# Kernel optimization log

Measured on AMD Instinct MI355X. Metric: run time of the kernel, lower is better.

Reference implementation:

```python
import jax, jax.numpy as jnp
import numpy as np

D_MODEL = 1024
D_STATE = 16
D_CONV = 4
EXPAND = 2
D_INNER = EXPAND * D_MODEL          # 2048
DT_RANK = D_INNER // 16             # 128
BATCH = 2
SEQLEN = 1024


def _silu(x):
    return x * jax.nn.sigmoid(x)


def setup_inputs() -> dict:
    key = jax.random.key(0)
    ks = jax.random.split(key, 8)
    s = 0.02
    A_init = jnp.tile(jnp.arange(1, D_STATE + 1, dtype=jnp.float32)[None, :], (D_INNER, 1))
    return {
        "x": jax.random.normal(ks[0], (BATCH, SEQLEN, D_MODEL), jnp.float32),
        "W_in": jax.random.normal(ks[1], (D_MODEL, 2 * D_INNER), jnp.float32) * s,
        "conv_k": jax.random.normal(ks[2], (D_CONV, 1, D_INNER), jnp.float32) * s,  # (kw, in/groups, out)
        "conv_b": jnp.zeros((D_INNER,), jnp.float32),
        "W_xproj": jax.random.normal(ks[3], (D_INNER, DT_RANK + 2 * D_STATE), jnp.float32) * s,
        "W_dt": jax.random.normal(ks[4], (DT_RANK, D_INNER), jnp.float32) * s,
        "b_dt": jnp.zeros((D_INNER,), jnp.float32),
        "A_log": jnp.log(A_init),
        "D": jnp.ones((D_INNER,), jnp.float32),
        "W_out": jax.random.normal(ks[5], (D_INNER, D_MODEL), jnp.float32) * s,
    }


def reference(x, W_in, conv_k, conv_b, W_xproj, W_dt, b_dt, A_log, D, W_out):
    # in_proj and gate split
    xz = x @ W_in                                   # (B, L, 2*Di)
    x_in, z = jnp.split(xz, 2, axis=-1)             # each (B, L, Di)

    # depthwise causal conv1d: left-pad by d_conv-1 (keras padding='causal')
    xp = jnp.pad(x_in, ((0, 0), (D_CONV - 1, 0), (0, 0)))
    x_in = jax.lax.conv_general_dilated(
        xp, conv_k, window_strides=(1,), padding='VALID',
        dimension_numbers=('NWC', 'WIO', 'NWC'),
        feature_group_count=D_INNER) + conv_b
    u = _silu(x_in)                                 # (B, L, Di)

    # input-dependent SSM params
    x_dbl = u @ W_xproj                             # (B, L, dt_rank + 2*N)
    dt_low, Bm, Cm = jnp.split(x_dbl, [DT_RANK, DT_RANK + D_STATE], axis=-1)
    dt = jax.nn.softplus(dt_low @ W_dt + b_dt)      # (B, L, Di)
    A = -jnp.exp(A_log)                             # (Di, N)
    dA = jnp.exp(jnp.einsum('bld,dn->bldn', dt, A)) # (B, L, Di, N)
    dB = jnp.einsum('bld,bln->bldn', dt, Bm)        # (B, L, Di, N)

    # selective scan over sequence length
    def step(h, e):
        a_t, b_t, u_t, c_t = e                      # (B,Di,N), (B,Di,N), (B,Di), (B,N)
        h = a_t * h + b_t * u_t[..., None]
        y_t = jnp.einsum('bdn,bn->bd', h, c_t)
        return h, y_t

    h0 = jnp.zeros((x.shape[0], D_INNER, D_STATE), dtype=x.dtype)
    xs = (jnp.swapaxes(dA, 0, 1), jnp.swapaxes(dB, 0, 1),
          jnp.swapaxes(u, 0, 1), jnp.swapaxes(Cm, 0, 1))
    _, yT = jax.lax.scan(step, h0, xs)              # (L, B, Di)
    y = jnp.swapaxes(yT, 0, 1) + u * D              # skip connection

    return (y * _silu(z)) @ W_out                   # (B, L, d_model)
```

## Files before the change

kernel.cpp:

```cpp
#include <hip/hip_runtime.h>
#include <hip/hip_bf16.h>

#define D_MODEL 1024
#define D_STATE 16
#define D_CONV 4
#define D_INNER 2048
#define DT_RANK 128
#define BATCH 2
#define SEQLEN 1024
#define XCOLS 160
#define NCHUNK 64
#define LCHUNK 16

typedef __hip_bfloat16 bf16;
typedef __attribute__((ext_vector_type(8))) short short8;
typedef __attribute__((ext_vector_type(4))) float f32x4;

__device__ __forceinline__ unsigned short f2bf_bits(float f) {
    bf16 h = __float2bfloat16(f);
    return *(unsigned short*)&h;
}

__device__ __forceinline__ float softplus_f(float x) {
    return fmaxf(x, 0.f) + __logf(1.f + __expf(-fabsf(x)));
}

__device__ __forceinline__ void load16_lds(void* lds, const void* g) {
    __builtin_amdgcn_global_load_lds(
        (const __attribute__((address_space(1))) unsigned int*)g,
        (__attribute__((address_space(3))) unsigned int*)lds, 16, 0, 0);
}

__device__ __forceinline__ void transpose_tile(const float* __restrict__ B,
                                               bf16* __restrict__ Bt,
                                               int K, int N, int nt, int kt,
                                               float (*t)[33], int tid)
{
    const int tx = tid & 31, ty = tid >> 5;
    const int n0 = nt * 32, k0 = kt * 32;
    #pragma unroll
    for (int r = 0; r < 4; ++r) {
        int n = n0 + tx;
        t[ty + r * 8][tx] = (n < N) ? B[(size_t)(k0 + ty + r * 8) * N + n] : 0.f;
    }
    __syncthreads();
    #pragma unroll
    for (int r = 0; r < 4; ++r)
        Bt[(size_t)(n0 + ty + r * 8) * K + k0 + tx] = __float2bfloat16(t[tx][ty + r * 8]);
}

__global__ __launch_bounds__(256)
void prep_kernel(const float* __restrict__ x, bf16* __restrict__ x_bf,
                 const float* __restrict__ W_in, bf16* __restrict__ Win_t,
                 const float* __restrict__ W_xproj, bf16* __restrict__ Wxp_t,
                 const float* __restrict__ W_dt, bf16* __restrict__ Wdt_t,
                 const float* __restrict__ W_out, bf16* __restrict__ Wout_t,
                 const float* __restrict__ A_log, float* __restrict__ Aneg)
{
    __shared__ float t[32][33];
    const int tid = threadIdx.x;
    int blk = blockIdx.x;
    if (blk < 4096) {
        transpose_tile(W_in, Win_t, D_MODEL, 2 * D_INNER, blk & 127, blk >> 7, t, tid);
        return;
    }
    blk -= 4096;
    if (blk < 512) {
        transpose_tile(W_xproj, Wxp_t, D_INNER, XCOLS, blk & 7, blk >> 3, t, tid);
        return;
    }
    blk -= 512;
    if (blk < 256) {
        transpose_tile(W_dt, Wdt_t, DT_RANK, D_INNER, blk & 63, blk >> 6, t, tid);
        return;
    }
    blk -= 256;
    if (blk < 2048) {
        transpose_tile(W_out, Wout_t, D_INNER, D_MODEL, blk & 31, blk >> 5, t, tid);
        return;
    }
    blk -= 2048;
    if (blk < 2048) {
        int i = blk * 256 + tid;
        float4 v = ((const float4*)x)[i];
        ushort4 p;
        p.x = f2bf_bits(v.x); p.y = f2bf_bits(v.y);
        p.z = f2bf_bits(v.z); p.w = f2bf_bits(v.w);
        ((ushort4*)x_bf)[i] = p;
        return;
    }
    blk -= 2048;
    {
        int i = blk * 256 + tid;
        Aneg[i] = -__expf(A_log[i]);
    }
}

template<int BN, int EPI>
__global__ __launch_bounds__(256)
void gemm_mfma(const bf16* __restrict__ A, const bf16* __restrict__ Bt,
               float* __restrict__ C, bf16* __restrict__ Cb,
               const float* __restrict__ bias,
               int M, int N, int K, int ldc, int kchunk)
{
    constexpr int WN = (BN == 128) ? 64 : 32;
    constexpr int NJ = WN / 16;
    __shared__ short As[128 * 32];
    __shared__ short Bs[BN * 32];
    const int tid = threadIdx.x;
    const int lane = tid & 63, wave = tid >> 6;
    const int wm = (wave >> 1) * 64, wn = (wave & 1) * WN;
    const int row0 = blockIdx.y * 128, col0 = blockIdx.x * BN;
    const int r_m = lane & 15, r_q = lane >> 4;
    const int kstart = blockIdx.z * kchunk;
    float* Cz = C + (size_t)blockIdx.z * M * ldc;

    const int srow = tid >> 2, schk = (tid & 3) * 8;
    const bf16* Ag0 = A  + (size_t)(row0 + srow)      * K + kstart + schk;
    const bf16* Ag1 = A  + (size_t)(row0 + srow + 64) * K + kstart + schk;
    const bf16* Bg0 = Bt + (size_t)(col0 + srow)      * K + kstart + schk;
    const bf16* Bg1 = Bt + (size_t)(col0 + srow + 64) * K + kstart + schk;
    short* AsW0 = &As[8 * tid];
    short* AsW1 = &As[8 * tid + 2048];
    short* BsW0 = &Bs[8 * tid];
    short* BsW1 = &Bs[8 * tid + 2048];

    f32x4 acc[4][NJ];
    #pragma unroll
    for (int i = 0; i < 4; ++i)
        #pragma unroll
        for (int j = 0; j < NJ; ++j)
            #pragma unroll
            for (int r = 0; r < 4; ++r) acc[i][j][r] = 0.f;

    for (int k0 = 0; k0 < kchunk; k0 += 32) {
        __syncthreads();
        load16_lds(AsW0, Ag0 + k0);
        load16_lds(AsW1, Ag1 + k0);
        load16_lds(BsW0, Bg0 + k0);
        if (BN == 128) load16_lds(BsW1, Bg1 + k0);
        __syncthreads();
        short8 af[4], bfr[NJ];
        #pragma unroll
        for (int i = 0; i < 4; ++i)
            af[i] = *(const short8*)&As[(wm + i * 16 + r_m) * 32 + r_q * 8];
        #pragma unroll
        for (int j = 0; j < NJ; ++j)
            bfr[j] = *(const short8*)&Bs[(wn + j * 16 + r_m) * 32 + r_q * 8];
        #pragma unroll
        for (int i = 0; i < 4; ++i)
            #pragma unroll
            for (int j = 0; j < NJ; ++j)
                acc[i][j] = __builtin_amdgcn_mfma_f32_16x16x32_bf16(
                    af[i], bfr[j], acc[i][j], 0, 0, 0);
    }

    #pragma unroll
    for (int i = 0; i < 4; ++i) {
        #pragma unroll
        for (int j = 0; j < NJ; ++j) {
            int row = row0 + wm + i * 16 + r_q * 4;
            int col = col0 + wn + j * 16 + r_m;
            if (col < N) {
                if (EPI == 1) {
                    float bv = bias[col];
                    #pragma unroll
                    for (int r = 0; r < 4; ++r)
                        Cb[(size_t)(row + r) * ldc + col] =
                            __float2bfloat16(softplus_f(acc[i][j][r] + bv));
                } else {
                    #pragma unroll
                    for (int r = 0; r < 4; ++r)
                        Cz[(size_t)(row + r) * ldc + col] = acc[i][j][r];
                }
            }
        }
    }
}

__global__ __launch_bounds__(256)
void reduce_xdbl(const float* __restrict__ Cpart, float* __restrict__ x_dbl,
                 bf16* __restrict__ dtA_bf)
{
    int i = blockIdx.x * 256 + threadIdx.x;
    if (i >= 2048 * XCOLS) return;
    int r = i / XCOLS, c = i - r * XCOLS;
    float s = 0.f;
    #pragma unroll
    for (int z = 0; z < 8; ++z)
        s += Cpart[(size_t)z * 2048 * 256 + (size_t)r * 256 + c];
    x_dbl[i] = s;
    if (c < DT_RANK) dtA_bf[(size_t)r * DT_RANK + c] = __float2bfloat16(s);
}

__global__ __launch_bounds__(256)
void reduce_out(const float* __restrict__ Cpart, float* __restrict__ out)
{
    int i = blockIdx.x * 256 + threadIdx.x;
    const float4* p0 = (const float4*)Cpart;
    const float4* p1 = p0 + (size_t)2048 * 1024 / 4;
    float4 a = p0[i], b = p1[i];
    float4 r; r.x = a.x + b.x; r.y = a.y + b.y; r.z = a.z + b.z; r.w = a.w + b.w;
    ((float4*)out)[i] = r;
}

__global__ __launch_bounds__(256)
void conv_silu_kernel(const float* __restrict__ xz,
                      const float* __restrict__ conv_k,
                      const float* __restrict__ conv_b,
                      bf16* __restrict__ u_bf)
{
    int idx4 = blockIdx.x * 256 + threadIdx.x;
    int d4 = idx4 & (D_INNER / 4 - 1);
    int t = (idx4 >> 9) & (SEQLEN - 1);
    int b = idx4 >> 19;
    float4 acc = ((const float4*)conv_b)[d4];
    #pragma unroll
    for (int k = 0; k < D_CONV; ++k) {
        int tt = t + k - (D_CONV - 1);
        if (tt >= 0) {
            float4 xv = ((const float4*)xz)[(size_t)(b * SEQLEN + tt) * (2 * D_INNER / 4) + d4];
            float4 kv = ((const float4*)conv_k)[k * (D_INNER / 4) + d4];
            acc.x = fmaf(xv.x, kv.x, acc.x);
            acc.y = fmaf(xv.y, kv.y, acc.y);
            acc.z = fmaf(xv.z, kv.z, acc.z);
            acc.w = fmaf(xv.w, kv.w, acc.w);
        }
    }
    ushort4 pk;
    pk.x = f2bf_bits(acc.x / (1.f + __expf(-acc.x)));
    pk.y = f2bf_bits(acc.y / (1.f + __expf(-acc.y)));
    pk.z = f2bf_bits(acc.z / (1.f + __expf(-acc.z)));
    pk.w = f2bf_bits(acc.w / (1.f + __expf(-acc.w)));
    ((ushort4*)u_bf)[idx4] = pk;
}

__global__ __launch_bounds__(256)
void scan_phase1(const bf16* __restrict__ dt_sb,
                 const float* __restrict__ Aneg,
                 const bf16* __restrict__ u_bf,
                 const float* __restrict__ x_dbl,
                 float* __restrict__ Pst, float* __restrict__ Sst)
{
    __shared__ float Bsm[LCHUNK][16];
    const int d = blockIdx.x * 256 + threadIdx.x;
    const int c = blockIdx.y, b = blockIdx.z;
    const int t0 = c * LCHUNK;
    {
        int tt = threadIdx.x >> 4, n = threadIdx.x & 15;
        Bsm[tt][n] = x_dbl[(size_t)(b * SEQLEN + t0 + tt) * XCOLS + DT_RANK + n];
    }
    float A_row[D_STATE];
    const float4* a4 = (const float4*)(Aneg + d * D_STATE);
    #pragma unroll
    for (int q = 0; q < 4; ++q) {
        float4 v = a4[q];
        A_row[q*4+0] = v.x; A_row[q*4+1] = v.y; A_row[q*4+2] = v.z; A_row[q*4+3] = v.w;
    }
    __syncthreads();
    float P[D_STATE], S[D_STATE];
    #pragma unroll
    for (int n = 0; n < D_STATE; ++n) { P[n] = 1.f; S[n] = 0.f; }
    const bf16* dpp = dt_sb + (size_t)(b * SEQLEN + t0) * D_INNER + d;
    const bf16* upp = u_bf + (size_t)(b * SEQLEN + t0) * D_INNER + d;
    #pragma unroll
    for (int t = 0; t < LCHUNK; ++t) {
        float dtv = __bfloat162float(dpp[(size_t)t * D_INNER]);
        float du = dtv * __bfloat162float(upp[(size_t)t * D_INNER]);
        const float4* b4 = (const float4*)&Bsm[t][0];
        #pragma unroll
        for (int q = 0; q < 4; ++q) {
            float4 v = b4[q];
            float Bn[4] = {v.x, v.y, v.z, v.w};
            #pragma unroll
            for (int e = 0; e < 4; ++e) {
                int n = q * 4 + e;
                float a = __expf(dtv * A_row[n]);
                P[n] *= a;
                S[n] = fmaf(a, S[n], du * Bn[e]);
            }
        }
    }
    const size_t base = ((size_t)(b * NCHUNK + c) * D_STATE) * D_INNER + d;
    #pragma unroll
    for (int n = 0; n < D_STATE; ++n) {
        Pst[base + (size_t)n * D_INNER] = P[n];
        Sst[base + (size_t)n * D_INNER] = S[n];
    }
}

__global__ __launch_bounds__(256)
void scan_phase2(const float* __restrict__ Pst, float* __restrict__ Sst)
{
    const int d = blockIdx.x * 256 + threadIdx.x;
    const int n = blockIdx.y;
    const int b = blockIdx.z;
    float h = 0.f;
    for (int c = 0; c < NCHUNK; ++c) {
        const size_t idx = ((size_t)(b * NCHUNK + c) * D_STATE + n) * D_INNER + d;
        float Pv = Pst[idx], Sv = Sst[idx];
        Sst[idx] = h;
        h = fmaf(Pv, h, Sv);
    }
}

__global__ __launch_bounds__(256)
void scan_phase3(const bf16* __restrict__ dt_sb,
                 const float* __restrict__ Aneg,
                 const bf16* __restrict__ u_bf,
                 const float* __restrict__ x_dbl,
                 const float* __restrict__ Dvec,
                 const float* __restrict__ xz,
                 const float* __restrict__ hin,
                 bf16* __restrict__ g_bf)
{
    __shared__ float BCs[LCHUNK][32];
    const int d = blockIdx.x * 256 + threadIdx.x;
    const int c = blockIdx.y, b = blockIdx.z;
    const int t0 = c * LCHUNK;
    {
        int i0 = threadIdx.x;
        int tt = i0 >> 5, col = i0 & 31;
        BCs[tt][col] = x_dbl[(size_t)(b * SEQLEN + t0 + tt) * XCOLS + DT_RANK + col];
        int i1 = i0 + 256;
        tt = i1 >> 5; col = i1 & 31;
        BCs[tt][col] = x_dbl[(size_t)(b * SEQLEN + t0 + tt) * XCOLS + DT_RANK + col];
    }
    float A_row[D_STATE];
    const float4* a4 = (const float4*)(Aneg + d * D_STATE);
    #pragma unroll
    for (int q = 0; q < 4; ++q) {
        float4 v = a4[q];
        A_row[q*4+0] = v.x; A_row[q*4+1] = v.y; A_row[q*4+2] = v.z; A_row[q*4+3] = v.w;
    }
    const float Dd = Dvec[d];
    __syncthreads();
    float h[D_STATE];
    const size_t base = ((size_t)(b * NCHUNK + c) * D_STATE) * D_INNER + d;
    #pragma unroll
    for (int n = 0; n < D_STATE; ++n) h[n] = hin[base + (size_t)n * D_INNER];
    const bf16* dpp = dt_sb + (size_t)(b * SEQLEN + t0) * D_INNER + d;
    const bf16* upp = u_bf + (size_t)(b * SEQLEN + t0) * D_INNER + d;
    const float* zpp = xz + (size_t)(b * SEQLEN + t0) * (2 * D_INNER) + D_INNER + d;
    bf16* gpp = g_bf + (size_t)(b * SEQLEN + t0) * D_INNER + d;
    #pragma unroll
    for (int t = 0; t < LCHUNK; ++t) {
        float dtv = __bfloat162float(dpp[(size_t)t * D_INNER]);
        float uv = __bfloat162float(upp[(size_t)t * D_INNER]);
        float zv = zpp[(size_t)t * 2 * D_INNER];
        float du = dtv * uv;
        float y = 0.f;
        const float4* bc4 = (const float4*)&BCs[t][0];
        #pragma unroll
        for (int q = 0; q < 4; ++q) {
            float4 v = bc4[q];
            float4 w = bc4[q + 4];
            float Bn[4] = {v.x, v.y, v.z, v.w};
            float Cn[4] = {w.x, w.y, w.z, w.w};
            #pragma unroll
            for (int e = 0; e < 4; ++e) {
                int n = q * 4 + e;
                float a = __expf(dtv * A_row[n]);
                h[n] = fmaf(a, h[n], du * Bn[e]);
                y = fmaf(h[n], Cn[e], y);
            }
        }
        float gy = y + uv * Dd;
        float sz = zv / (1.f + __expf(-zv));
        gpp[(size_t)t * D_INNER] = __float2bfloat16(gy * sz);
    }
}

extern "C" void kernel_launch(void* const* d_in, const int* in_sizes, int n_in,
                              void* d_out, int out_size, void* d_ws, size_t ws_size,
                              hipStream_t stream)
{
    const float* x      = (const float*)d_in[0];
    const float* W_in   = (const float*)d_in[1];
    const float* conv_k = (const float*)d_in[2];
    const float* conv_b = (const float*)d_in[3];
    const float* W_xproj= (const float*)d_in[4];
    const float* W_dt   = (const float*)d_in[5];
    const float* b_dt   = (const float*)d_in[6];
    const float* A_log  = (const float*)d_in[7];
    const float* Dvec   = (const float*)d_in[8];
    const float* W_out  = (const float*)d_in[9];
    float* out = (float*)d_out;

    const int BL = BATCH * SEQLEN;

    float* ws     = (float*)d_ws;
    float* xz     = ws;
    float* x_dbl  = xz     + (size_t)BL * 2 * D_INNER;
    float* Pst    = x_dbl  + (size_t)BL * XCOLS;
    float* Sst    = Pst    + (size_t)BATCH * NCHUNK * D_STATE * D_INNER;
    float* Aneg   = Sst    + (size_t)BATCH * NCHUNK * D_STATE * D_INNER;
    float* Cpart3 = Pst;
    float* Cpart6 = Pst;
    bf16*  x_bf   = (bf16*)Sst;
    bf16* Win_t  = (bf16*)(Aneg + 32768);
    bf16* u_bf   = Win_t + (size_t)4096 * 1024;
    bf16* Wxp_t  = u_bf  + (size_t)BL * D_INNER;
    bf16* dtA_bf = Wxp_t + (size_t)256 * 2048;
    bf16* Wdt_t  = dtA_bf+ (size_t)BL * DT_RANK;
    bf16* g_bf   = Wdt_t + (size_t)2048 * 128;
    bf16* Wout_t = g_bf  + (size_t)BL * D_INNER;
    bf16* dt_sb  = Wout_t+ (size_t)1024 * 2048;

    prep_kernel<<<4096 + 512 + 256 + 2048 + 2048 + 128, 256, 0, stream>>>(
        x, x_bf, W_in, Win_t, W_xproj, Wxp_t, W_dt, Wdt_t, W_out, Wout_t, A_log, Aneg);

    gemm_mfma<128, 0><<<dim3(32, 16, 1), 256, 0, stream>>>(
        x_bf, Win_t, xz, nullptr, nullptr, BL, 2 * D_INNER, D_MODEL, 2 * D_INNER, D_MODEL);

    conv_silu_kernel<<<(BL * D_INNER / 4) / 256, 256, 0, stream>>>(xz, conv_k, conv_b, u_bf);

    gemm_mfma<64, 0><<<dim3(4, 16, 8), 256, 0, stream>>>(
        u_bf, Wxp_t, Cpart3, nullptr, nullptr, BL, 256, D_INNER, 256, 256);
    reduce_xdbl<<<(BL * XCOLS + 255) / 256, 256, 0, stream>>>(Cpart3, x_dbl, dtA_bf);

    gemm_mfma<64, 1><<<dim3(32, 16, 1), 256, 0, stream>>>(
        dtA_bf, Wdt_t, nullptr, dt_sb, b_dt, BL, D_INNER, DT_RANK, D_INNER, DT_RANK);

    scan_phase1<<<dim3(D_INNER / 256, NCHUNK, BATCH), 256, 0, stream>>>(
        dt_sb, Aneg, u_bf, x_dbl, Pst, Sst);
    scan_phase2<<<dim3(D_INNER / 256, D_STATE, BATCH), 256, 0, stream>>>(Pst, Sst);
    scan_phase3<<<dim3(D_INNER / 256, NCHUNK, BATCH), 256, 0, stream>>>(
        dt_sb, Aneg, u_bf, x_dbl, Dvec, xz, Sst, g_bf);

    gemm_mfma<64, 0><<<dim3(16, 16, 2), 256, 0, stream>>>(
        g_bf, Wout_t, Cpart6, nullptr, nullptr, BL, D_MODEL, D_INNER, D_MODEL, D_MODEL);
    reduce_out<<<(BL * D_MODEL / 4) / 256, 256, 0, stream>>>(Cpart6, out);
}
```

Before: 234.7 us.

## Fuse z-gate SiLU into in_proj epilogue and retune scan chunks and split-K

```diff
diff --git a/kernel.cpp b/kernel.cpp
--- a/kernel.cpp
+++ b/kernel.cpp
@@ -9,8 +9,8 @@
 #define BATCH 2
 #define SEQLEN 1024
 #define XCOLS 160
-#define NCHUNK 64
-#define LCHUNK 16
+#define NCHUNK 32
+#define LCHUNK 32
 
 typedef __hip_bfloat16 bf16;
 typedef __attribute__((ext_vector_type(8))) short short8;
@@ -23,6 +23,10 @@
 
 __device__ __forceinline__ float softplus_f(float x) {
     return fmaxf(x, 0.f) + __logf(1.f + __expf(-fabsf(x)));
+}
+
+__device__ __forceinline__ float silu_f(float x) {
+    return x / (1.f + __expf(-x));
 }
 
 __device__ __forceinline__ void load16_lds(void* lds, const void* g) {
@@ -168,6 +172,18 @@
                     for (int r = 0; r < 4; ++r)
                         Cb[(size_t)(row + r) * ldc + col] =
                             __float2bfloat16(softplus_f(acc[i][j][r] + bv));
+                } else if (EPI == 2) {
+                    if (col < 2048) {
+                        #pragma unroll
+                        for (int r = 0; r < 4; ++r)
+                            Cz[(size_t)(row + r) * ldc + col] = acc[i][j][r];
+                    } else {
+                        int zc = col - 2048;
+                        #pragma unroll
+                        for (int r = 0; r < 4; ++r)
+                            Cb[(size_t)(row + r) * ldc + zc] =
+                                __float2bfloat16(silu_f(acc[i][j][r]));
+                    }
                 } else {
                     #pragma unroll
                     for (int r = 0; r < 4; ++r)
@@ -197,15 +213,19 @@
 void reduce_out(const float* __restrict__ Cpart, float* __restrict__ out)
 {
     int i = blockIdx.x * 256 + threadIdx.x;
-    const float4* p0 = (const float4*)Cpart;
-    const float4* p1 = p0 + (size_t)2048 * 1024 / 4;
-    float4 a = p0[i], b = p1[i];
-    float4 r; r.x = a.x + b.x; r.y = a.y + b.y; r.z = a.z + b.z; r.w = a.w + b.w;
+    const size_t stride = (size_t)2048 * 1024 / 4;
+    const float4* p = (const float4*)Cpart;
+    float4 a = p[i], b = p[i + stride], c = p[i + 2 * stride], d = p[i + 3 * stride];
+    float4 r;
+    r.x = (a.x + b.x) + (c.x + d.x);
+    r.y = (a.y + b.y) + (c.y + d.y);
+    r.z = (a.z + b.z) + (c.z + d.z);
+    r.w = (a.w + b.w) + (c.w + d.w);
     ((float4*)out)[i] = r;
 }
 
 __global__ __launch_bounds__(256)
-void conv_silu_kernel(const float* __restrict__ xz,
+void conv_silu_kernel(const float* __restrict__ x_lin,
                       const float* __restrict__ conv_k,
                       const float* __restrict__ conv_b,
                       bf16* __restrict__ u_bf)
@@ -219,7 +239,7 @@
     for (int k = 0; k < D_CONV; ++k) {
         int tt = t + k - (D_CONV - 1);
         if (tt >= 0) {
-            float4 xv = ((const float4*)xz)[(size_t)(b * SEQLEN + tt) * (2 * D_INNER / 4) + d4];
+            float4 xv = ((const float4*)x_lin)[(size_t)(b * SEQLEN + tt) * (D_INNER / 4) + d4];
             float4 kv = ((const float4*)conv_k)[k * (D_INNER / 4) + d4];
             acc.x = fmaf(xv.x, kv.x, acc.x);
             acc.y = fmaf(xv.y, kv.y, acc.y);
@@ -246,8 +266,8 @@
     const int d = blockIdx.x * 256 + threadIdx.x;
     const int c = blockIdx.y, b = blockIdx.z;
     const int t0 = c * LCHUNK;
-    {
-        int tt = threadIdx.x >> 4, n = threadIdx.x & 15;
+    for (int i = threadIdx.x; i < LCHUNK * 16; i += 256) {
+        int tt = i >> 4, n = i & 15;
         Bsm[tt][n] = x_dbl[(size_t)(b * SEQLEN + t0 + tt) * XCOLS + DT_RANK + n];
     }
     float A_row[D_STATE];
@@ -263,7 +283,7 @@
     for (int n = 0; n < D_STATE; ++n) { P[n] = 1.f; S[n] = 0.f; }
     const bf16* dpp = dt_sb + (size_t)(b * SEQLEN + t0) * D_INNER + d;
     const bf16* upp = u_bf + (size_t)(b * SEQLEN + t0) * D_INNER + d;
-    #pragma unroll
+    #pragma unroll 8
     for (int t = 0; t < LCHUNK; ++t) {
         float dtv = __bfloat162float(dpp[(size_t)t * D_INNER]);
         float du = dtv * __bfloat162float(upp[(size_t)t * D_INNER]);
@@ -310,7 +330,7 @@
                  const bf16* __restrict__ u_bf,
                  const float* __restrict__ x_dbl,
                  const float* __restrict__ Dvec,
-                 const float* __restrict__ xz,
+                 const bf16* __restrict__ sz_bf,
                  const float* __restrict__ hin,
                  bf16* __restrict__ g_bf)
 {
@@ -318,12 +338,8 @@
     const int d = blockIdx.x * 256 + threadIdx.x;
     const int c = blockIdx.y, b = blockIdx.z;
     const int t0 = c * LCHUNK;
-    {
-        int i0 = threadIdx.x;
-        int tt = i0 >> 5, col = i0 & 31;
-        BCs[tt][col] = x_dbl[(size_t)(b * SEQLEN + t0 + tt) * XCOLS + DT_RANK + col];
-        int i1 = i0 + 256;
-        tt = i1 >> 5; col = i1 & 31;
+    for (int i = threadIdx.x; i < LCHUNK * 32; i += 256) {
+        int tt = i >> 5, col = i & 31;
         BCs[tt][col] = x_dbl[(size_t)(b * SEQLEN + t0 + tt) * XCOLS + DT_RANK + col];
     }
     float A_row[D_STATE];
@@ -341,13 +357,13 @@
     for (int n = 0; n < D_STATE; ++n) h[n] = hin[base + (size_t)n * D_INNER];
     const bf16* dpp = dt_sb + (size_t)(b * SEQLEN + t0) * D_INNER + d;
     const bf16* upp = u_bf + (size_t)(b * SEQLEN + t0) * D_INNER + d;
-    const float* zpp = xz + (size_t)(b * SEQLEN + t0) * (2 * D_INNER) + D_INNER + d;
+    const bf16* zpp = sz_bf + (size_t)(b * SEQLEN + t0) * D_INNER + d;
     bf16* gpp = g_bf + (size_t)(b * SEQLEN + t0) * D_INNER + d;
-    #pragma unroll
+    #pragma unroll 8
     for (int t = 0; t < LCHUNK; ++t) {
         float dtv = __bfloat162float(dpp[(size_t)t * D_INNER]);
         float uv = __bfloat162float(upp[(size_t)t * D_INNER]);
-        float zv = zpp[(size_t)t * 2 * D_INNER];
+        float sz = __bfloat162float(zpp[(size_t)t * D_INNER]);
         float du = dtv * uv;
         float y = 0.f;
         const float4* bc4 = (const float4*)&BCs[t][0];
@@ -366,7 +382,6 @@
             }
         }
         float gy = y + uv * Dd;
-        float sz = zv / (1.f + __expf(-zv));
         gpp[(size_t)t * D_INNER] = __float2bfloat16(gy * sz);
     }
 }
@@ -390,17 +405,17 @@
     const int BL = BATCH * SEQLEN;
 
     float* ws     = (float*)d_ws;
-    float* xz     = ws;
-    float* x_dbl  = xz     + (size_t)BL * 2 * D_INNER;
-    float* Pst    = x_dbl  + (size_t)BL * XCOLS;
-    float* Sst    = Pst    + (size_t)BATCH * NCHUNK * D_STATE * D_INNER;
-    float* Aneg   = Sst    + (size_t)BATCH * NCHUNK * D_STATE * D_INNER;
-    float* Cpart3 = Pst;
-    float* Cpart6 = Pst;
-    bf16*  x_bf   = (bf16*)Sst;
-    bf16* Win_t  = (bf16*)(Aneg + 32768);
+    float* x_lin  = ws;
+    float* x_dbl  = x_lin + (size_t)BL * D_INNER;
+    float* Pst    = x_dbl + (size_t)BL * XCOLS;
+    float* Sst    = Pst + (size_t)BATCH * NCHUNK * D_STATE * D_INNER;
+    float* Aneg   = Sst + (size_t)BATCH * NCHUNK * D_STATE * D_INNER;
+    float* Cpart  = Aneg + 32768;
+    bf16*  x_bf   = (bf16*)Cpart;
+    bf16* Win_t  = (bf16*)(Cpart + (size_t)4 * 2048 * 1024);
     bf16* u_bf   = Win_t + (size_t)4096 * 1024;
-    bf16* Wxp_t  = u_bf  + (size_t)BL * D_INNER;
+    bf16* sz_bf  = u_bf  + (size_t)BL * D_INNER;
+    bf16* Wxp_t  = sz_bf + (size_t)BL * D_INNER;
     bf16* dtA_bf = Wxp_t + (size_t)256 * 2048;
     bf16* Wdt_t  = dtA_bf+ (size_t)BL * DT_RANK;
     bf16* g_bf   = Wdt_t + (size_t)2048 * 128;
@@ -410,14 +425,14 @@
     prep_kernel<<<4096 + 512 + 256 + 2048 + 2048 + 128, 256, 0, stream>>>(
         x, x_bf, W_in, Win_t, W_xproj, Wxp_t, W_dt, Wdt_t, W_out, Wout_t, A_log, Aneg);
 
-    gemm_mfma<128, 0><<<dim3(32, 16, 1), 256, 0, stream>>>(
-        x_bf, Win_t, xz, nullptr, nullptr, BL, 2 * D_INNER, D_MODEL, 2 * D_INNER, D_MODEL);
-
-    conv_silu_kernel<<<(BL * D_INNER / 4) / 256, 256, 0, stream>>>(xz, conv_k, conv_b, u_bf);
-
-    gemm_mfma<64, 0><<<dim3(4, 16, 8), 256, 0, stream>>>(
-        u_bf, Wxp_t, Cpart3, nullptr, nullptr, BL, 256, D_INNER, 256, 256);
-    reduce_xdbl<<<(BL * XCOLS + 255) / 256, 256, 0, stream>>>(Cpart3, x_dbl, dtA_bf);
+    gemm_mfma<128, 2><<<dim3(32, 16, 1), 256, 0, stream>>>(
+        x_bf, Win_t, x_lin, sz_bf, nullptr, BL, 2 * D_INNER, D_MODEL, D_INNER, D_MODEL);
+
+    conv_silu_kernel<<<(BL * D_INNER / 4) / 256, 256, 0, stream>>>(x_lin, conv_k, conv_b, u_bf);
+
+    gemm_mfma<64, 0><<<dim3(3, 16, 8), 256, 0, stream>>>(
+        u_bf, Wxp_t, Cpart, nullptr, nullptr, BL, 256, D_INNER, 256, 256);
+    reduce_xdbl<<<(BL * XCOLS + 255) / 256, 256, 0, stream>>>(Cpart, x_dbl, dtA_bf);
 
     gemm_mfma<64, 1><<<dim3(32, 16, 1), 256, 0, stream>>>(
         dtA_bf, Wdt_t, nullptr, dt_sb, b_dt, BL, D_INNER, DT_RANK, D_INNER, DT_RANK);
@@ -426,9 +441,9 @@
         dt_sb, Aneg, u_bf, x_dbl, Pst, Sst);
     scan_phase2<<<dim3(D_INNER / 256, D_STATE, BATCH), 256, 0, stream>>>(Pst, Sst);
     scan_phase3<<<dim3(D_INNER / 256, NCHUNK, BATCH), 256, 0, stream>>>(
-        dt_sb, Aneg, u_bf, x_dbl, Dvec, xz, Sst, g_bf);
-
-    gemm_mfma<64, 0><<<dim3(16, 16, 2), 256, 0, stream>>>(
-        g_bf, Wout_t, Cpart6, nullptr, nullptr, BL, D_MODEL, D_INNER, D_MODEL, D_MODEL);
-    reduce_out<<<(BL * D_MODEL / 4) / 256, 256, 0, stream>>>(Cpart6, out);
-}
+        dt_sb, Aneg, u_bf, x_dbl, Dvec, sz_bf, Sst, g_bf);
+
+    gemm_mfma<128, 0><<<dim3(8, 16, 4), 256, 0, stream>>>(
+        g_bf, Wout_t, Cpart, nullptr, nullptr, BL, D_MODEL, D_INNER, D_MODEL, D_INNER / 4);
+    reduce_out<<<(BL * D_MODEL / 4) / 256, 256, 0, stream>>>(Cpart, out);
+}
```

Measured after the change: 255.7 us. +8.9%, slower.
